# Performance work log

Measured on AMD Instinct MI355X. Metric: run time of the kernel, lower is better.

## Reference

```python
import jax, jax.numpy as jnp
import numpy as np

TEMP = 0.05
EPS = 0.1  # label smoothing epsilon (cfg.MODEL.LOSSES.CE.EPSILON)

B, D, N, P = 256, 2048, 65536, 4096


def setup_inputs() -> dict:
    key = jax.random.key(0)
    k1, k2, k3, k4 = jax.random.split(key, 4)
    inputs = jax.random.normal(k1, (B, D), dtype=jnp.float32)
    targets = jax.random.randint(k2, (B,), 0, N)
    prototype = jax.random.normal(k3, (B, P), dtype=jnp.float32)
    features = jax.random.normal(k4, (N, D), dtype=jnp.float32)
    # memory bank rows are kept L2-normalized by the EMA update rule
    features = features / jnp.linalg.norm(features, axis=1, keepdims=True)
    return {"inputs": inputs, "targets": targets, "prototype": prototype, "features": features}


def reference(inputs, targets, prototype, features):
    # F.normalize(inputs, dim=1)
    x = inputs / jnp.linalg.norm(inputs, axis=1, keepdims=True)
    # CM.forward: inputs.mm(features.t())
    mem_logits = x @ features.T                     # [B, N]
    logits = jnp.concatenate([prototype / TEMP, mem_logits / TEMP], axis=1)  # [B, P+N]
    targets_all = targets + prototype.shape[1]
    # label-smoothed cross entropy
    logp = jax.nn.log_softmax(logits, axis=1)       # [B, P+N]
    num_classes = logits.shape[1]
    nll = -jnp.take_along_axis(logp, targets_all[:, None], axis=1)[:, 0]  # [B]
    smooth = -logp.mean(axis=1)                     # [B]
    loss = jnp.mean((1.0 - EPS) * nll + EPS * smooth)
    return loss
```

## Files before the change

### kernel.cpp

```cpp
#include <hip/hip_runtime.h>
#include <stdint.h>

#define M_ROWS 256
#define K_DIM  2048
#define N_FEAT 65536
#define P_PROTO 4096
#define INV_T  20.0f
#define N_CLS  69632.0f

typedef __attribute__((ext_vector_type(8))) __bf16 bf16x8;
typedef __attribute__((ext_vector_type(4))) float  f32x4;

__device__ __forceinline__ unsigned short f2bf_rne(float f) {
    unsigned int u = __float_as_uint(f);
    u += 0x7fffu + ((u >> 16) & 1u);
    return (unsigned short)(u >> 16);
}

__global__ __launch_bounds__(256) void prep_norm(const float* __restrict__ in,
                                                 unsigned short* __restrict__ xb) {
    const int row = blockIdx.x;
    const int tid = threadIdx.x;
    const float4* r = (const float4*)(in + (size_t)row * K_DIM);
    float4 v0 = r[tid];
    float4 v1 = r[tid + 256];
    float ss = v0.x*v0.x + v0.y*v0.y + v0.z*v0.z + v0.w*v0.w
             + v1.x*v1.x + v1.y*v1.y + v1.z*v1.z + v1.w*v1.w;
    #pragma unroll
    for (int off = 32; off; off >>= 1) ss += __shfl_down(ss, off, 64);
    __shared__ float wsum[4];
    if ((tid & 63) == 0) wsum[tid >> 6] = ss;
    __syncthreads();
    float scale = rsqrtf(wsum[0] + wsum[1] + wsum[2] + wsum[3]);

    ushort4 o0, o1;
    o0.x = f2bf_rne(v0.x * scale); o0.y = f2bf_rne(v0.y * scale);
    o0.z = f2bf_rne(v0.z * scale); o0.w = f2bf_rne(v0.w * scale);
    o1.x = f2bf_rne(v1.x * scale); o1.y = f2bf_rne(v1.y * scale);
    o1.z = f2bf_rne(v1.z * scale); o1.w = f2bf_rne(v1.w * scale);
    ushort4* o = (ushort4*)(xb + (size_t)row * K_DIM);
    o[tid]       = o0;
    o[tid + 256] = o1;
}

#define BK 32
#define NT 64

__global__ __launch_bounds__(256) void gemm_nt(const unsigned short* __restrict__ xb,
                                               const float* __restrict__ feat,
                                               float* __restrict__ C) {
    __shared__ unsigned short lA[M_ROWS * BK];
    __shared__ unsigned short lB[NT * BK];

    const int tid = threadIdx.x;
    const int w   = tid >> 6;
    const int l   = tid & 63;
    const int lr  = l & 15;
    const int lq  = l >> 4;
    const int n0  = blockIdx.x * NT;

    const unsigned short* agp = xb + (size_t)(w * 64 + (l >> 2)) * K_DIM + (l & 3) * 8;
    const int bn = tid >> 2;
    const int bc = tid & 3;
    const float* fptr = feat + (size_t)(n0 + bn) * K_DIM + bc * 8;
    unsigned short* lbdst = lB + bn * BK + bc * 8;

    const unsigned short* aptr = lA + (size_t)((w * 4) * 16 + lr) * BK + lq * 8;
    const unsigned short* bptr = lB + (size_t)lr * BK + lq * 8;

    f32x4 acc[4][4];
    #pragma unroll
    for (int i = 0; i < 4; ++i)
        #pragma unroll
        for (int j = 0; j < 4; ++j)
            acc[i][j] = (f32x4){0.f, 0.f, 0.f, 0.f};

    for (int kt = 0; kt < K_DIM / BK; ++kt) {
        __syncthreads();
        #pragma unroll
        for (int t = 0; t < 4; ++t) {
            __builtin_amdgcn_global_load_lds(
                (const __attribute__((address_space(1))) void*)(agp + (size_t)t * 16 * K_DIM),
                (__attribute__((address_space(3))) void*)((char*)lA + w * 4096 + t * 1024),
                16, 0, 0);
        }
        float4 f0 = *(const float4*)(fptr);
        float4 f1 = *(const float4*)(fptr + 4);
        uint4 pk;
        pk.x = (unsigned)f2bf_rne(f0.x) | ((unsigned)f2bf_rne(f0.y) << 16);
        pk.y = (unsigned)f2bf_rne(f0.z) | ((unsigned)f2bf_rne(f0.w) << 16);
        pk.z = (unsigned)f2bf_rne(f1.x) | ((unsigned)f2bf_rne(f1.y) << 16);
        pk.w = (unsigned)f2bf_rne(f1.z) | ((unsigned)f2bf_rne(f1.w) << 16);
        *(uint4*)lbdst = pk;
        agp  += BK;
        fptr += BK;
        __syncthreads();

        bf16x8 a[4], b[4];
        #pragma unroll
        for (int i = 0; i < 4; ++i) a[i] = *(const bf16x8*)(aptr + (size_t)i * 16 * BK);
        #pragma unroll
        for (int j = 0; j < 4; ++j) b[j] = *(const bf16x8*)(bptr + (size_t)j * 16 * BK);
        #pragma unroll
        for (int i = 0; i < 4; ++i)
            #pragma unroll
            for (int j = 0; j < 4; ++j)
                acc[i][j] = __builtin_amdgcn_mfma_f32_16x16x32_bf16(a[i], b[j], acc[i][j], 0, 0, 0);
    }

    #pragma unroll
    for (int i = 0; i < 4; ++i) {
        const int mbase = (w * 4 + i) * 16 + lq * 4;
        #pragma unroll
        for (int j = 0; j < 4; ++j) {
            const int col = n0 + j * 16 + lr;
            #pragma unroll
            for (int r = 0; r < 4; ++r)
                C[(size_t)(mbase + r) * N_FEAT + col] = acc[i][j][r];
        }
    }
}

__device__ __forceinline__ void online_lse(float v, float& m, float& s) {
    if (v > m) { s = s * __expf(m - v) + 1.0f; m = v; }
    else       { s += __expf(v - m); }
}

__global__ __launch_bounds__(256) void row_reduce(const float* __restrict__ proto,
                                                  const float* __restrict__ C,
                                                  const int* __restrict__ targets,
                                                  float* __restrict__ rowvals) {
    const int row = blockIdx.x;
    const int tid = threadIdx.x;
    const float* p = proto + (size_t)row * P_PROTO;
    const float* c = C + (size_t)row * N_FEAT;

    float m = -1.0e30f, s = 0.0f, sum = 0.0f;

    const float4* p4 = (const float4*)p;
    for (int i = tid; i < P_PROTO / 4; i += 256) {
        float4 v = p4[i];
        float a0 = v.x * INV_T, a1 = v.y * INV_T, a2 = v.z * INV_T, a3 = v.w * INV_T;
        sum += a0 + a1 + a2 + a3;
        online_lse(a0, m, s); online_lse(a1, m, s);
        online_lse(a2, m, s); online_lse(a3, m, s);
    }
    const float4* c4 = (const float4*)c;
    for (int i = tid; i < N_FEAT / 4; i += 256) {
        float4 v = c4[i];
        float a0 = v.x * INV_T, a1 = v.y * INV_T, a2 = v.z * INV_T, a3 = v.w * INV_T;
        sum += a0 + a1 + a2 + a3;
        online_lse(a0, m, s); online_lse(a1, m, s);
        online_lse(a2, m, s); online_lse(a3, m, s);
    }

    __shared__ float rm[256], rs[256], rsum[256];
    rm[tid] = m; rs[tid] = s; rsum[tid] = sum;
    __syncthreads();
    #pragma unroll
    for (int off = 128; off; off >>= 1) {
        if (tid < off) {
            float m2 = rm[tid + off], s2 = rs[tid + off];
            float mn = fmaxf(rm[tid], m2);
            rs[tid] = rs[tid] * __expf(rm[tid] - mn) + s2 * __expf(m2 - mn);
            rm[tid] = mn;
            rsum[tid] += rsum[tid + off];
        }
        __syncthreads();
    }
    if (tid == 0) {
        const int t = targets[row];
        const float lt = c[t] * INV_T;
        const float lse = rm[0] + __logf(rs[0]);
        rowvals[row] = lse - 0.9f * lt - 0.1f * (rsum[0] / N_CLS);
    }
}

__global__ __launch_bounds__(256) void final_mean(const float* __restrict__ rowvals,
                                                  float* __restrict__ out) {
    const int tid = threadIdx.x;
    float v = rowvals[tid];
    #pragma unroll
    for (int off = 32; off; off >>= 1) v += __shfl_down(v, off, 64);
    __shared__ float ws[4];
    if ((tid & 63) == 0) ws[tid >> 6] = v;
    __syncthreads();
    if (tid == 0) out[0] = (ws[0] + ws[1] + ws[2] + ws[3]) * (1.0f / 256.0f);
}

extern "C" void kernel_launch(void* const* d_in, const int* in_sizes, int n_in,
                              void* d_out, int out_size, void* d_ws, size_t ws_size,
                              hipStream_t stream) {
    const float* inputs  = (const float*)d_in[0];
    const int*   targets = (const int*)d_in[1];
    const float* proto   = (const float*)d_in[2];
    const float* feat    = (const float*)d_in[3];

    unsigned short* xb = (unsigned short*)d_ws;
    float* C       = (float*)((char*)d_ws + (size_t)M_ROWS * K_DIM * 2);
    float* rowvals = (float*)((char*)C + (size_t)M_ROWS * N_FEAT * 4);
    float* out     = (float*)d_out;

    prep_norm <<<M_ROWS, 256, 0, stream>>>(inputs, xb);
    gemm_nt   <<<N_FEAT / NT, 256, 0, stream>>>(xb, feat, C);
    row_reduce<<<M_ROWS, 256, 0, stream>>>(proto, C, targets, rowvals);
    final_mean<<<1, 256, 0, stream>>>(rowvals, out);
}
```

Baseline: 784.9 us.

## Fuse log-sum-exp partial reduction into GEMM epilogue, drop full logits matrix

The GEMM epilogue now reduces each 64-column tile to a per-row partial max, sum of exponentials and sum of logits, instead of writing the full 256x65536 fp32 logits matrix. A new small kernel computes the target logit directly as a bf16-rounded dot product. The final row kernel merges the 1024 partials per row plus the prototype logits. This removes a 64 MB write and the matching re-read, and replaces the serial per-element online softmax with a block-wise merge. In exchange the epilogue does extra shuffles and exponentials, and the target logit is computed in a different summation order than the MFMA path.

```diff
diff --git a/kernel.cpp b/kernel.cpp
--- a/kernel.cpp
+++ b/kernel.cpp
@@ -7,6 +7,9 @@
 #define P_PROTO 4096
 #define INV_T  20.0f
 #define N_CLS  69632.0f
+#define BK 32
+#define NT 64
+#define NBLK (N_FEAT / NT)
 
 typedef __attribute__((ext_vector_type(8))) __bf16 bf16x8;
 typedef __attribute__((ext_vector_type(4))) float  f32x4;
@@ -15,6 +18,9 @@
     unsigned int u = __float_as_uint(f);
     u += 0x7fffu + ((u >> 16) & 1u);
     return (unsigned short)(u >> 16);
+}
+__device__ __forceinline__ float bf2f(unsigned short u) {
+    return __uint_as_float(((unsigned int)u) << 16);
 }
 
 __global__ __launch_bounds__(256) void prep_norm(const float* __restrict__ in,
@@ -43,12 +49,38 @@
     o[tid + 256] = o1;
 }
 
-#define BK 32
-#define NT 64
-
-__global__ __launch_bounds__(256) void gemm_nt(const unsigned short* __restrict__ xb,
-                                               const float* __restrict__ feat,
-                                               float* __restrict__ C) {
+__global__ __launch_bounds__(256) void tdot(const unsigned short* __restrict__ xb,
+                                            const float* __restrict__ feat,
+                                            const int* __restrict__ targets,
+                                            float* __restrict__ td) {
+    const int row = blockIdx.x;
+    const int tid = threadIdx.x;
+    const int t = targets[row];
+    const ushort4* xr = (const ushort4*)(xb + (size_t)row * K_DIM);
+    const float4*  fr = (const float4*)(feat + (size_t)t * K_DIM);
+    ushort4 xa = xr[tid * 2], xc = xr[tid * 2 + 1];
+    float4  fa = fr[tid * 2], fc = fr[tid * 2 + 1];
+    float d = bf2f(xa.x) * bf2f(f2bf_rne(fa.x))
+            + bf2f(xa.y) * bf2f(f2bf_rne(fa.y))
+            + bf2f(xa.z) * bf2f(f2bf_rne(fa.z))
+            + bf2f(xa.w) * bf2f(f2bf_rne(fa.w))
+            + bf2f(xc.x) * bf2f(f2bf_rne(fc.x))
+            + bf2f(xc.y) * bf2f(f2bf_rne(fc.y))
+            + bf2f(xc.z) * bf2f(f2bf_rne(fc.z))
+            + bf2f(xc.w) * bf2f(f2bf_rne(fc.w));
+    #pragma unroll
+    for (int off = 32; off; off >>= 1) d += __shfl_down(d, off, 64);
+    __shared__ float ws[4];
+    if ((tid & 63) == 0) ws[tid >> 6] = d;
+    __syncthreads();
+    if (tid == 0) td[row] = ws[0] + ws[1] + ws[2] + ws[3];
+}
+
+__global__ __launch_bounds__(256) void gemm_fused(const unsigned short* __restrict__ xb,
+                                                  const float* __restrict__ feat,
+                                                  float* __restrict__ Pm,
+                                                  float* __restrict__ Ps,
+                                                  float* __restrict__ Psum) {
     __shared__ unsigned short lA[M_ROWS * BK];
     __shared__ unsigned short lB[NT * BK];
 
@@ -110,48 +142,65 @@
 
     #pragma unroll
     for (int i = 0; i < 4; ++i) {
-        const int mbase = (w * 4 + i) * 16 + lq * 4;
-        #pragma unroll
-        for (int j = 0; j < 4; ++j) {
-            const int col = n0 + j * 16 + lr;
+        #pragma unroll
+        for (int r = 0; r < 4; ++r) {
+            float v0 = acc[i][0][r] * INV_T;
+            float v1 = acc[i][1][r] * INV_T;
+            float v2 = acc[i][2][r] * INV_T;
+            float v3 = acc[i][3][r] * INV_T;
+            float mx = fmaxf(fmaxf(v0, v1), fmaxf(v2, v3));
             #pragma unroll
-            for (int r = 0; r < 4; ++r)
-                C[(size_t)(mbase + r) * N_FEAT + col] = acc[i][j][r];
+            for (int msk = 1; msk < 16; msk <<= 1)
+                mx = fmaxf(mx, __shfl_xor(mx, msk, 16));
+            float s  = __expf(v0 - mx) + __expf(v1 - mx) + __expf(v2 - mx) + __expf(v3 - mx);
+            float sm = v0 + v1 + v2 + v3;
+            #pragma unroll
+            for (int msk = 1; msk < 16; msk <<= 1) {
+                s  += __shfl_xor(s,  msk, 16);
+                sm += __shfl_xor(sm, msk, 16);
+            }
+            if (lr == 0) {
+                const int row = (w * 4 + i) * 16 + lq * 4 + r;
+                const size_t idx = (size_t)row * NBLK + blockIdx.x;
+                Pm[idx] = mx; Ps[idx] = s; Psum[idx] = sm;
+            }
         }
     }
 }
 
-__device__ __forceinline__ void online_lse(float v, float& m, float& s) {
-    if (v > m) { s = s * __expf(m - v) + 1.0f; m = v; }
-    else       { s += __expf(v - m); }
-}
-
-__global__ __launch_bounds__(256) void row_reduce(const float* __restrict__ proto,
-                                                  const float* __restrict__ C,
-                                                  const int* __restrict__ targets,
-                                                  float* __restrict__ rowvals) {
+__global__ __launch_bounds__(256) void row_final(const float* __restrict__ proto,
+                                                 const float* __restrict__ Pm,
+                                                 const float* __restrict__ Ps,
+                                                 const float* __restrict__ Psum,
+                                                 const float* __restrict__ td,
+                                                 float* __restrict__ rowvals) {
     const int row = blockIdx.x;
     const int tid = threadIdx.x;
-    const float* p = proto + (size_t)row * P_PROTO;
-    const float* c = C + (size_t)row * N_FEAT;
-
     float m = -1.0e30f, s = 0.0f, sum = 0.0f;
 
-    const float4* p4 = (const float4*)p;
-    for (int i = tid; i < P_PROTO / 4; i += 256) {
-        float4 v = p4[i];
+    const float* pm = Pm   + (size_t)row * NBLK;
+    const float* ps = Ps   + (size_t)row * NBLK;
+    const float* pu = Psum + (size_t)row * NBLK;
+    #pragma unroll
+    for (int k = 0; k < NBLK / 256; ++k) {
+        const int b = tid + k * 256;
+        float mb = pm[b], sb = ps[b];
+        float nm = fmaxf(m, mb);
+        s = s * __expf(m - nm) + sb * __expf(mb - nm);
+        m = nm;
+        sum += pu[b];
+    }
+    const float4* p4 = (const float4*)(proto + (size_t)row * P_PROTO);
+    #pragma unroll
+    for (int k = 0; k < P_PROTO / 4 / 256; ++k) {
+        float4 v = p4[tid + k * 256];
         float a0 = v.x * INV_T, a1 = v.y * INV_T, a2 = v.z * INV_T, a3 = v.w * INV_T;
+        float lm = fmaxf(fmaxf(a0, a1), fmaxf(a2, a3));
+        float nm = fmaxf(m, lm);
+        s = s * __expf(m - nm)
+          + __expf(a0 - nm) + __expf(a1 - nm) + __expf(a2 - nm) + __expf(a3 - nm);
+        m = nm;
         sum += a0 + a1 + a2 + a3;
-        online_lse(a0, m, s); online_lse(a1, m, s);
-        online_lse(a2, m, s); online_lse(a3, m, s);
-    }
-    const float4* c4 = (const float4*)c;
-    for (int i = tid; i < N_FEAT / 4; i += 256) {
-        float4 v = c4[i];
-        float a0 = v.x * INV_T, a1 = v.y * INV_T, a2 = v.z * INV_T, a3 = v.w * INV_T;
-        sum += a0 + a1 + a2 + a3;
-        online_lse(a0, m, s); online_lse(a1, m, s);
-        online_lse(a2, m, s); online_lse(a3, m, s);
     }
 
     __shared__ float rm[256], rs[256], rsum[256];
@@ -161,17 +210,16 @@
     for (int off = 128; off; off >>= 1) {
         if (tid < off) {
             float m2 = rm[tid + off], s2 = rs[tid + off];
-            float mn = fmaxf(rm[tid], m2);
-            rs[tid] = rs[tid] * __expf(rm[tid] - mn) + s2 * __expf(m2 - mn);
-            rm[tid] = mn;
+            float nm = fmaxf(rm[tid], m2);
+            rs[tid] = rs[tid] * __expf(rm[tid] - nm) + s2 * __expf(m2 - nm);
+            rm[tid] = nm;
             rsum[tid] += rsum[tid + off];
         }
         __syncthreads();
     }
     if (tid == 0) {
-        const int t = targets[row];
-        const float lt = c[t] * INV_T;
         const float lse = rm[0] + __logf(rs[0]);
+        const float lt  = td[row] * INV_T;
         rowvals[row] = lse - 0.9f * lt - 0.1f * (rsum[0] / N_CLS);
     }
 }
@@ -196,13 +244,18 @@
     const float* proto   = (const float*)d_in[2];
     const float* feat    = (const float*)d_in[3];
 
-    unsigned short* xb = (unsigned short*)d_ws;
-    float* C       = (float*)((char*)d_ws + (size_t)M_ROWS * K_DIM * 2);
-    float* rowvals = (float*)((char*)C + (size_t)M_ROWS * N_FEAT * 4);
+    char* ws = (char*)d_ws;
+    unsigned short* xb = (unsigned short*)ws;
+    float* Pm      = (float*)(ws + (1u << 20));
+    float* Ps      = (float*)(ws + (2u << 20));
+    float* Psum    = (float*)(ws + (3u << 20));
+    float* td      = (float*)(ws + (4u << 20));
+    float* rowvals = (float*)(ws + (4u << 20) + 4096);
     float* out     = (float*)d_out;
 
     prep_norm <<<M_ROWS, 256, 0, stream>>>(inputs, xb);
-    gemm_nt   <<<N_FEAT / NT, 256, 0, stream>>>(xb, feat, C);
-    row_reduce<<<M_ROWS, 256, 0, stream>>>(proto, C, targets, rowvals);
-    final_mean<<<1, 256, 0, stream>>>(rowvals, out);
-}
+    tdot      <<<M_ROWS, 256, 0, stream>>>(xb, feat, targets, td);
+    gemm_fused<<<NBLK,   256, 0, stream>>>(xb, feat, Pm, Ps, Psum);
+    row_final <<<M_ROWS, 256, 0, stream>>>(proto, Pm, Ps, Psum, td, rowvals);
+    final_mean<<<1,      256, 0, stream>>>(rowvals, out);
+}
```

New measurement: 794.3 us. No clear change (+1.2%).
